# Performance work log

Hardware: AMD Instinct MI355X
Metric: run time of the kernel (lower is better)

Reference implementation:

```python
import jax, jax.numpy as jnp
import numpy as np

KERNEL = 5
STRIDE = 1
DN = ('NHWC', 'HWIO', 'NHWC')
PRIOR_VAR = 0.01


def setup_inputs() -> dict:
    key = jax.random.key(0)
    k1, k2, k3 = jax.random.split(key, 3)
    mu_in = jax.random.normal(k1, (32, 224, 224, 3), dtype=jnp.float32)
    # GlorotNormal-ish scale for a 5x5x3 -> 64 kernel
    w_mu = jax.random.normal(k2, (5, 5, 3, 64), dtype=jnp.float32) * 0.12
    # original init: uniform in [min_sigma, ini_sigma] = [-4.6, -2.25]
    w_sigma = jax.random.uniform(k3, (64,), dtype=jnp.float32, minval=-4.6, maxval=-2.25)
    return {"mu_in": mu_in, "w_mu": w_mu, "w_sigma": w_sigma}


def reference(mu_in, w_mu, w_sigma):
    # KL regularizer: broadcast of (64,) logvar against (5,5,3,64) mu, mean over all
    kl = 0.5 * jnp.mean(
        jnp.log(PRIOR_VAR) - 1.0 - w_sigma
        + jax.nn.softplus(w_sigma) / PRIOR_VAR
        + jnp.square(w_mu) / PRIOR_VAR
    )

    w_sigma_2 = jax.nn.softplus(w_sigma)  # log(1+exp(w_sigma))

    # Mean path: standard conv2d, VALID, stride 1, NHWC
    mu_out = jax.lax.conv_general_dilated(
        mu_in, w_mu, (STRIDE, STRIDE), 'VALID', dimension_numbers=DN
    )  # [B, Ho, Wo, K]

    # Variance path: per-output-location sum over the k*k*C patch of x^2 / x_dim.
    # Same math as the original extract_patches + reduce_sum, but computed as a
    # channel-summed box filter on x^2 (no im2col materialization).
    C = mu_in.shape[-1]
    x_dim = jnp.asarray(KERNEL * KERNEL * C, mu_in.dtype)
    ones_k = jnp.ones((KERNEL, KERNEL, C, 1), mu_in.dtype)
    sq = jax.lax.conv_general_dilated(
        jnp.square(mu_in), ones_k, (STRIDE, STRIDE), 'VALID', dimension_numbers=DN
    ) / x_dim  # [B, Ho, Wo, 1]

    Sigma_out = jax.nn.softplus(w_sigma_2 * sq)  # broadcast -> [B, Ho, Wo, K]
    return (mu_out, Sigma_out, kl)
```

## Files before the change

kernel.cpp:

```cpp
#include <hip/hip_runtime.h>
#include <math.h>

#define BATCH 32
#define HIN   224
#define WIN   224
#define CIN   3
#define KOUT  64
#define RK    5
#define HOUT  220
#define WOUT  220

#define TH     16
#define TW     32
#define PATCH_H (TH + RK - 1)
#define PATCH_W (TW + RK - 1)
#define SROW_F  112
#define NTOT ((size_t)BATCH * HOUT * WOUT * KOUT)

typedef float  v4f    __attribute__((ext_vector_type(4)));
typedef short  short8 __attribute__((ext_vector_type(8)));

#define WS_WF_FRAGS 768
#define WS_WSG_OFF  12288

__device__ __forceinline__ float exp2_hw(float x) { float r; asm("v_exp_f32 %0, %1" : "=v"(r) : "v"(x)); return r; }
__device__ __forceinline__ float log2_hw(float x) { float r; asm("v_log_f32 %0, %1" : "=v"(r) : "v"(x)); return r; }
#define LOG2E 1.44269504088896f
#define LN2   0.69314718055995f

__device__ __forceinline__ float softplus_hw(float x) {
    float t = exp2_hw(-fabsf(x) * LOG2E);
    return fmaxf(x, 0.0f) + LN2 * log2_hw(1.0f + t);
}
__device__ __forceinline__ float softplus_pos(float y) {
    return y + LN2 * log2_hw(1.0f + exp2_hw(-y * LOG2E));
}
__device__ __forceinline__ short f2bf(float x) {
    unsigned u = __float_as_uint(x);
    u = (u + 0x7FFFu + ((u >> 16) & 1u)) >> 16;
    return (short)u;
}

__global__ __launch_bounds__(256) void vdp_prep_kernel(
    const float* __restrict__ w_mu, const float* __restrict__ w_sigma,
    void* __restrict__ ws, float* __restrict__ out)
{
    __shared__ float red[4];
    short8* wf = (short8*)ws;
    float* wsg = (float*)((char*)ws + WS_WSG_OFF);
    const int t = threadIdx.x;

    for (int f = t; f < WS_WF_FRAGS; f += 256) {
        const int s  = f >> 8;
        const int nb = (f >> 6) & 3;
        const int l  = f & 63;
        const int ch = nb * 16 + (l & 15);
        const int h2 = l >> 4;
        short8 r;
        #pragma unroll
        for (int i = 0; i < 8; ++i) {
            const int k = s * 32 + h2 * 8 + i;
            const int kh = k >> 4, inner = k & 15;
            float v = 0.0f;
            if (inner < 15 && k < 80) {
                const int kw = inner / 3;
                const int c  = inner - kw * 3;
                v = w_mu[((kh * 5 + kw) * 3 + c) * KOUT + ch];
            }
            r[i] = f2bf(v);
        }
        wf[f] = r;
    }
    if (t < KOUT) wsg[t] = softplus_hw(w_sigma[t]);

    float s = 0.0f;
    for (int i = t; i < RK * RK * CIN * KOUT; i += 256) {
        const float v = w_mu[i];
        s = fmaf(v, v, s);
    }
    float u = s * (100.0f / 4800.0f);
    if (t < KOUT) {
        const float wsv = w_sigma[t];
        u += (-wsv + softplus_hw(wsv) * 100.0f) * (1.0f / 64.0f);
    }
    #pragma unroll
    for (int off = 32; off > 0; off >>= 1)
        u += __shfl_down(u, off, 64);
    if ((t & 63) == 0) red[t >> 6] = u;
    __syncthreads();
    if (t == 0) {
        const float U = red[0] + red[1] + red[2] + red[3];
        out[2 * NTOT] = 0.5f * (-4.6051701860f - 1.0f + U);
    }
}

__global__ __launch_bounds__(256, 4) void vdp_conv_kernel(
    const float* __restrict__ mu_in, const void* __restrict__ ws, float* __restrict__ out)
{
    __shared__ float s_row[PATCH_H][SROW_F];
    __shared__ float s_ssq[PATCH_H][40];
    __shared__ float s_sq[TH][TW];

    const int tid  = threadIdx.x;
    const int lane = tid & 63;
    const int wid  = tid >> 6;
    const int p    = lane & 15;
    const int h2   = lane >> 4;

    const int b = blockIdx.z;
    int ho0 = blockIdx.y * TH; if (ho0 > HOUT - TH) ho0 = HOUT - TH;
    int wo0 = blockIdx.x * TW; if (wo0 > WOUT - TW) wo0 = WOUT - TW;

    const short8* wfg = (const short8*)ws;
    short8 wf[12];
    #pragma unroll
    for (int f = 0; f < 12; ++f) wf[f] = wfg[f * 64 + lane];
    const float* wsg_g = (const float*)((const char*)ws + WS_WSG_OFF);
    const v4f wsg_kg = *(const v4f*)(wsg_g + p * 4);

    const size_t inbase = ((size_t)b * HIN + ho0) * (WIN * CIN) + wo0 * CIN;
    for (int idx = tid; idx < PATCH_H * SROW_F; idx += 256) {
        const int r = idx / SROW_F, c = idx - r * SROW_F;
        float v = 0.0f;
        if (c < PATCH_W * CIN) v = mu_in[inbase + (size_t)r * (WIN * CIN) + c];
        s_row[r][c] = v;
    }
    __syncthreads();

    for (int idx = tid; idx < PATCH_H * PATCH_W; idx += 256) {
        const int r = idx / PATCH_W, px = idx - r * PATCH_W;
        const float a0 = s_row[r][3 * px], a1 = s_row[r][3 * px + 1], a2 = s_row[r][3 * px + 2];
        s_ssq[r][px] = fmaf(a0, a0, fmaf(a1, a1, a2 * a2));
    }
    __syncthreads();

    #pragma unroll
    for (int h = 0; h < 2; ++h) {
        const int orow = (tid >> 5) + h * 8, pc = tid & 31;
        float a = 0.0f;
        #pragma unroll
        for (int kh = 0; kh < RK; ++kh)
            #pragma unroll
            for (int kw = 0; kw < RK; ++kw)
                a += s_ssq[orow + kh][pc + kw];
        s_sq[orow][pc] = a * (1.0f / 75.0f);
    }
    __syncthreads();

    #pragma unroll 1
    for (int j = 0; j < 4; ++j) {
        const int rt = (wid << 2) | j;
        const size_t rowbase = (((size_t)b * HOUT + ho0 + rt) * WOUT + wo0) * KOUT;

        #pragma unroll
        for (int g = 0; g < 2; ++g) {
            short8 pf[3];
            #pragma unroll
            for (int s = 0; s < 3; ++s) {
                int ridx = rt + 2 * s + (h2 >> 1);
                ridx = ridx > PATCH_H - 1 ? PATCH_H - 1 : ridx;
                const float* rp = &s_row[ridx][3 * (16 * g + p) + 8 * (h2 & 1)];
                short8 r;
                #pragma unroll
                for (int i = 0; i < 8; ++i) r[i] = f2bf(rp[i]);
                pf[s] = r;
            }
            v4f acc[4];
            #pragma unroll
            for (int nb = 0; nb < 4; ++nb) {
                v4f a = {0.0f, 0.0f, 0.0f, 0.0f};
                #pragma unroll
                for (int s = 0; s < 3; ++s)
                    a = __builtin_amdgcn_mfma_f32_16x16x32_bf16(wf[s * 4 + nb], pf[s], a, 0, 0, 0);
                acc[nb] = a;
            }
            float* mp = out + rowbase + (size_t)(16 * g + p) * KOUT + h2 * 4;
            #pragma unroll
            for (int nb = 0; nb < 4; ++nb)
                *(v4f*)(mp + nb * 16) = acc[nb];
        }

        float* sp = out + NTOT + rowbase + p * 4;
        #pragma unroll
        for (int q = 0; q < 8; ++q) {
            const int px = (q << 2) | h2;
            const float sq = s_sq[rt][px];
            v4f sg;
            sg.x = softplus_pos(wsg_kg.x * sq);
            sg.y = softplus_pos(wsg_kg.y * sq);
            sg.z = softplus_pos(wsg_kg.z * sq);
            sg.w = softplus_pos(wsg_kg.w * sq);
            *(v4f*)(sp + (size_t)px * KOUT) = sg;
        }
    }
}

extern "C" void kernel_launch(void* const* d_in, const int* in_sizes, int n_in,
                              void* d_out, int out_size, void* d_ws, size_t ws_size,
                              hipStream_t stream)
{
    (void)in_sizes; (void)n_in; (void)ws_size; (void)out_size;
    const float* mu_in   = (const float*)d_in[0];
    const float* w_mu    = (const float*)d_in[1];
    const float* w_sigma = (const float*)d_in[2];
    float* out = (float*)d_out;

    vdp_prep_kernel<<<1, 256, 0, stream>>>(w_mu, w_sigma, d_ws, out);
    dim3 grid((WOUT + TW - 1) / TW, (HOUT + TH - 1) / TH, BATCH);
    vdp_conv_kernel<<<grid, 256, 0, stream>>>(mu_in, d_ws, out);
}
```

Baseline: 198.1 us.

## Split fused conv into separate mu and sigma kernels with full-row sigma tiles

Splits the single fused kernel into two launches: an MFMA kernel that writes only the mean output, and a separate sigma kernel. The sigma kernel loads full 224-wide input rows for four output rows per block and computes the box sum separably (vertical then horizontal). This removes overlapping tile recomputation and the idle store phases in the mu kernel. In exchange the input is read twice, the kernels launch serially, and the second kernel has few blocks, each writing a long row stream.

```diff
diff --git a/kernel.cpp b/kernel.cpp
--- a/kernel.cpp
+++ b/kernel.cpp
@@ -94,12 +94,10 @@
     }
 }
 
-__global__ __launch_bounds__(256, 4) void vdp_conv_kernel(
+__global__ __launch_bounds__(256, 4) void vdp_mu_kernel(
     const float* __restrict__ mu_in, const void* __restrict__ ws, float* __restrict__ out)
 {
     __shared__ float s_row[PATCH_H][SROW_F];
-    __shared__ float s_ssq[PATCH_H][40];
-    __shared__ float s_sq[TH][TW];
 
     const int tid  = threadIdx.x;
     const int lane = tid & 63;
@@ -115,8 +113,6 @@
     short8 wf[12];
     #pragma unroll
     for (int f = 0; f < 12; ++f) wf[f] = wfg[f * 64 + lane];
-    const float* wsg_g = (const float*)((const char*)ws + WS_WSG_OFF);
-    const v4f wsg_kg = *(const v4f*)(wsg_g + p * 4);
 
     const size_t inbase = ((size_t)b * HIN + ho0) * (WIN * CIN) + wo0 * CIN;
     for (int idx = tid; idx < PATCH_H * SROW_F; idx += 256) {
@@ -124,26 +120,6 @@
         float v = 0.0f;
         if (c < PATCH_W * CIN) v = mu_in[inbase + (size_t)r * (WIN * CIN) + c];
         s_row[r][c] = v;
-    }
-    __syncthreads();
-
-    for (int idx = tid; idx < PATCH_H * PATCH_W; idx += 256) {
-        const int r = idx / PATCH_W, px = idx - r * PATCH_W;
-        const float a0 = s_row[r][3 * px], a1 = s_row[r][3 * px + 1], a2 = s_row[r][3 * px + 2];
-        s_ssq[r][px] = fmaf(a0, a0, fmaf(a1, a1, a2 * a2));
-    }
-    __syncthreads();
-
-    #pragma unroll
-    for (int h = 0; h < 2; ++h) {
-        const int orow = (tid >> 5) + h * 8, pc = tid & 31;
-        float a = 0.0f;
-        #pragma unroll
-        for (int kh = 0; kh < RK; ++kh)
-            #pragma unroll
-            for (int kw = 0; kw < RK; ++kw)
-                a += s_ssq[orow + kh][pc + kw];
-        s_sq[orow][pc] = a * (1.0f / 75.0f);
     }
     __syncthreads();
 
@@ -179,19 +155,64 @@
             for (int nb = 0; nb < 4; ++nb)
                 *(v4f*)(mp + nb * 16) = acc[nb];
         }
-
-        float* sp = out + NTOT + rowbase + p * 4;
-        #pragma unroll
-        for (int q = 0; q < 8; ++q) {
-            const int px = (q << 2) | h2;
-            const float sq = s_sq[rt][px];
-            v4f sg;
-            sg.x = softplus_pos(wsg_kg.x * sq);
-            sg.y = softplus_pos(wsg_kg.y * sq);
-            sg.z = softplus_pos(wsg_kg.z * sq);
-            sg.w = softplus_pos(wsg_kg.w * sq);
-            *(v4f*)(sp + (size_t)px * KOUT) = sg;
-        }
+    }
+}
+
+__global__ __launch_bounds__(256, 4) void vdp_sigma_kernel(
+    const float* __restrict__ mu_in, const void* __restrict__ ws, float* __restrict__ out)
+{
+    __shared__ float s_row[8 * 672];
+    __shared__ float s_ssq[8][224];
+    __shared__ float s_cs[4][224];
+
+    const int tid  = threadIdx.x;
+    const int lane = tid & 63;
+    const int wid  = tid >> 6;
+    const int p    = lane & 15;
+    const int h2   = lane >> 4;
+
+    const int b  = blockIdx.y;
+    const int r0 = blockIdx.x * 4;
+
+    const float* wsg_g = (const float*)((const char*)ws + WS_WSG_OFF);
+    const v4f wsg_kg = *(const v4f*)(wsg_g + p * 4);
+
+    {
+        const v4f* gin = (const v4f*)(mu_in + ((size_t)b * HIN + r0) * (WIN * CIN));
+        v4f* dst = (v4f*)s_row;
+        for (int i = tid; i < 8 * 672 / 4; i += 256) dst[i] = gin[i];
+    }
+    __syncthreads();
+
+    for (int idx = tid; idx < 8 * 224; idx += 256) {
+        const int r = idx >> 5 >> 3;
+        const int rr = idx / 224, px = idx - rr * 224;
+        const float* q = &s_row[rr * 672 + 3 * px];
+        s_ssq[rr][px] = fmaf(q[0], q[0], fmaf(q[1], q[1], q[2] * q[2]));
+        (void)r;
+    }
+    __syncthreads();
+
+    for (int idx = tid; idx < 4 * 224; idx += 256) {
+        const int rr = idx / 224, px = idx - rr * 224;
+        s_cs[rr][px] = s_ssq[rr][px] + s_ssq[rr + 1][px] + s_ssq[rr + 2][px]
+                     + s_ssq[rr + 3][px] + s_ssq[rr + 4][px];
+    }
+    __syncthreads();
+
+    const int rt = wid;
+    float* sp = out + NTOT + (((size_t)b * HOUT + r0 + rt) * WOUT) * KOUT + p * 4;
+    #pragma unroll 1
+    for (int q = 0; q < 55; ++q) {
+        const int px = (q << 2) | h2;
+        const float sq = (s_cs[rt][px] + s_cs[rt][px + 1] + s_cs[rt][px + 2]
+                        + s_cs[rt][px + 3] + s_cs[rt][px + 4]) * (1.0f / 75.0f);
+        v4f sg;
+        sg.x = softplus_pos(wsg_kg.x * sq);
+        sg.y = softplus_pos(wsg_kg.y * sq);
+        sg.z = softplus_pos(wsg_kg.z * sq);
+        sg.w = softplus_pos(wsg_kg.w * sq);
+        *(v4f*)(sp + (size_t)px * KOUT) = sg;
     }
 }
 
@@ -206,6 +227,8 @@
     float* out = (float*)d_out;
 
     vdp_prep_kernel<<<1, 256, 0, stream>>>(w_mu, w_sigma, d_ws, out);
-    dim3 grid((WOUT + TW - 1) / TW, (HOUT + TH - 1) / TH, BATCH);
-    vdp_conv_kernel<<<grid, 256, 0, stream>>>(mu_in, d_ws, out);
-}
+    dim3 grid_mu((WOUT + TW - 1) / TW, (HOUT + TH - 1) / TH, BATCH);
+    vdp_mu_kernel<<<grid_mu, 256, 0, stream>>>(mu_in, d_ws, out);
+    dim3 grid_sg(HOUT / 4, BATCH, 1);
+    vdp_sigma_kernel<<<grid_sg, 256, 0, stream>>>(mu_in, d_ws, out);
+}
```

After: 200.1 us. Within noise of the previous version (+1.0%).
